# Performance work log

Hardware: AMD Instinct MI355X
Metric: run time of the kernel (lower is better)

The kernel has to match this reference:

```python
import jax, jax.numpy as jnp
import numpy as np

N, E, D, C = 50000, 800000, 128, 7
BN_EPS = 1e-5


def _sage_conv(x, src, dst, Wl, Wr, b):
    # mean-aggregate neighbor messages per destination, then linear + root linear
    msgs = x[src]  # [E, D] irregular gather
    summed = jax.ops.segment_sum(msgs, dst, num_segments=N)
    cnt = jax.ops.segment_sum(jnp.ones((src.shape[0],), x.dtype), dst, num_segments=N)
    agg = summed / jnp.maximum(cnt, 1.0)[:, None]
    return agg @ Wl.T + x @ Wr.T + b


def _bn_eval(x, g, be):
    # running_mean=0, running_var=1 (eval mode)
    return x * (g / jnp.sqrt(1.0 + BN_EPS)) + be


def setup_inputs() -> dict:
    key = jax.random.key(0)
    ks = jax.random.split(key, 20)
    w = lambda k, s: jax.random.normal(k, s, dtype=jnp.float32) * 0.05
    inp = {
        "x": jax.random.normal(ks[0], (N, D), dtype=jnp.float32),
        "edge_index": jax.random.randint(ks[1], (2, E), 0, N, dtype=jnp.int64),
        "Wl0": w(ks[2], (D, D)), "Wr0": w(ks[3], (D, D)), "b0": jnp.zeros((D,), jnp.float32),
        "Wl1": w(ks[4], (D, D)), "Wr1": w(ks[5], (D, D)), "b1": jnp.zeros((D,), jnp.float32),
        "Wl2": w(ks[6], (D, D)), "Wr2": w(ks[7], (D, D)), "b2": jnp.zeros((D,), jnp.float32),
        "g0": jnp.ones((D,), jnp.float32), "be0": jnp.zeros((D,), jnp.float32),
        "g1": jnp.ones((D,), jnp.float32), "be1": jnp.zeros((D,), jnp.float32),
        "dW1": w(ks[8], (D, D)), "db1": jnp.zeros((D,), jnp.float32),
        "dW2": w(ks[9], (C, D)), "db2": jnp.zeros((C,), jnp.float32),
        "dW3": w(ks[10], (D, D)), "db3": jnp.zeros((D,), jnp.float32),
    }
    return inp


def reference(x, edge_index, Wl0, Wr0, b0, Wl1, Wr1, b1, Wl2, Wr2, b2,
              g0, be0, g1, be1, dW1, db1, dW2, db2, dW3, db3):
    src, dst = edge_index[0], edge_index[1]
    h = _sage_conv(x, src, dst, Wl0, Wr0, b0)
    h = jax.nn.relu(_bn_eval(h, g0, be0))  # dropout is identity in eval
    h = _sage_conv(h, src, dst, Wl1, Wr1, b1)
    h = jax.nn.relu(_bn_eval(h, g1, be1))
    h = _sage_conv(h, src, dst, Wl2, Wr2, b2)
    recon_x1 = h @ dW1.T + db1
    recon_x2 = h @ dW2.T + db2
    recon_x3 = h @ dW3.T + db3
    return (recon_x1, recon_x2, recon_x3)
```

## Files before the change

kernel.cpp:

```cpp
#include <hip/hip_runtime.h>
#include <hip/hip_fp16.h>

static constexpr float kBnEps = 1e-5f;
static constexpr int MAXB = 1024;

typedef __attribute__((ext_vector_type(8))) _Float16 f16x8;
typedef __attribute__((ext_vector_type(4))) float f32x4;

__global__ void detect_k(const int* __restrict__ eb, int* __restrict__ flag) {
    int l = threadIdx.x;
    int v = eb[2 * l + 1];
    unsigned long long m = __ballot(v == 0);
    if (l == 0) flag[0] = (m == ~0ull) ? 1 : 0;
}

__device__ __forceinline__ int edge_src(const int* eb, int is64, int E, int e) {
    return is64 ? eb[2 * e] : eb[e];
}
__device__ __forceinline__ int edge_dst(const int* eb, int is64, int E, int e) {
    return is64 ? eb[2 * E + 2 * e] : eb[E + e];
}

__global__ __launch_bounds__(256) void histA_k(const int* __restrict__ eb,
                                               const int* __restrict__ flag,
                                               int* __restrict__ gcnt, int E,
                                               int nbuck) {
    __shared__ int lh[MAXB];
    for (int i = threadIdx.x; i < nbuck; i += 256) lh[i] = 0;
    __syncthreads();
    int is64 = flag[0];
    int base = blockIdx.x * 4096;
#pragma unroll
    for (int i = 0; i < 16; ++i) {
        int e = base + i * 256 + threadIdx.x;
        if (e < E) {
            int d = edge_dst(eb, is64, E, e);
            atomicAdd(&lh[d >> 7], 1);
        }
    }
    __syncthreads();
    for (int i = threadIdx.x; i < nbuck; i += 256) {
        int c = lh[i];
        if (c) atomicAdd(&gcnt[i], c);
    }
}

__global__ __launch_bounds__(512) void scanB_k(const int* __restrict__ gcnt,
                                               int* __restrict__ gbase,
                                               int* __restrict__ gcur,
                                               int* __restrict__ offs, int E,
                                               int n, int nbuck) {
    __shared__ int s[512];
    int tid = threadIdx.x;
    int v = (tid < nbuck) ? gcnt[tid] : 0;
    s[tid] = v;
    __syncthreads();
    for (int d = 1; d < 512; d <<= 1) {
        int t = (tid >= d) ? s[tid - d] : 0;
        __syncthreads();
        s[tid] += t;
        __syncthreads();
    }
    if (tid < nbuck) {
        gbase[tid] = s[tid] - v;
        gcur[tid] = s[tid] - v;
    }
    if (tid == 0) {
        gbase[nbuck] = E;
        offs[n] = E;
    }
}

__global__ __launch_bounds__(256) void binC_k(const int* __restrict__ eb,
                                              const int* __restrict__ flag,
                                              int* __restrict__ gcur,
                                              unsigned* __restrict__ bins, int E,
                                              int nbuck) {
    __shared__ int lh[MAXB];
    __shared__ int lcur[MAXB];
    for (int i = threadIdx.x; i < nbuck; i += 256) lh[i] = 0;
    __syncthreads();
    int is64 = flag[0];
    int base = blockIdx.x * 4096;
    int ds[16], ss[16];
#pragma unroll
    for (int i = 0; i < 16; ++i) {
        int e = base + i * 256 + threadIdx.x;
        ds[i] = -1;
        if (e < E) {
            ds[i] = edge_dst(eb, is64, E, e);
            ss[i] = edge_src(eb, is64, E, e);
            atomicAdd(&lh[ds[i] >> 7], 1);
        }
    }
    __syncthreads();
    for (int b = threadIdx.x; b < nbuck; b += 256) {
        int c = lh[b];
        lcur[b] = c ? atomicAdd(&gcur[b], c) : 0;
    }
    __syncthreads();
#pragma unroll
    for (int i = 0; i < 16; ++i) {
        if (ds[i] >= 0) {
            int bkt = ds[i] >> 7;
            int p = atomicAdd(&lcur[bkt], 1);
            bins[p] = ((unsigned)ss[i] << 7) | (unsigned)(ds[i] & 127);
        }
    }
}

__global__ __launch_bounds__(256) void csrD_k(const unsigned* __restrict__ bins,
                                              const int* __restrict__ gbase,
                                              int* __restrict__ offs,
                                              int* __restrict__ csr, int n) {
    int b = blockIdx.x;
    __shared__ int hist[128];
    __shared__ int s[128];
    __shared__ int cur[128];
    int tid = threadIdx.x;
    if (tid < 128) hist[tid] = 0;
    __syncthreads();
    int base = gbase[b], endb = gbase[b + 1], m = endb - base;
    for (int i = tid; i < m; i += 256) atomicAdd(&hist[bins[base + i] & 127u], 1);
    __syncthreads();
    int v = 0;
    if (tid < 128) {
        v = hist[tid];
        s[tid] = v;
    }
    __syncthreads();
    for (int d = 1; d < 128; d <<= 1) {
        int t = (tid >= d && tid < 128) ? s[tid - d] : 0;
        __syncthreads();
        if (tid < 128) s[tid] += t;
        __syncthreads();
    }
    if (tid < 128) {
        int excl = s[tid] - v;
        int dst = b * 128 + tid;
        if (dst < n) offs[dst] = base + excl;
        cur[tid] = base + excl;
    }
    __syncthreads();
    for (int i = tid; i < m; i += 256) {
        unsigned u = bins[base + i];
        int p = atomicAdd(&cur[u & 127u], 1);
        csr[p] = (int)(u >> 7);
    }
}

__global__ void cvtx_k(const float* __restrict__ in, __half* __restrict__ out, int total8) {
    int i = blockIdx.x * blockDim.x + threadIdx.x;
    if (i >= total8) return;
    float4 v0 = ((const float4*)in)[2 * i];
    float4 v1 = ((const float4*)in)[2 * i + 1];
    __half2 h0 = __floats2half2_rn(v0.x, v0.y);
    __half2 h1 = __floats2half2_rn(v0.z, v0.w);
    __half2 h2 = __floats2half2_rn(v1.x, v1.y);
    __half2 h3 = __floats2half2_rn(v1.z, v1.w);
    uint4 o;
    o.x = *(uint*)&h0; o.y = *(uint*)&h1; o.z = *(uint*)&h2; o.w = *(uint*)&h3;
    ((uint4*)out)[i] = o;
}

__global__ void cvtw_k(const float* __restrict__ Wl0, const float* __restrict__ Wr0,
                       const float* __restrict__ Wl1, const float* __restrict__ Wr1,
                       const float* __restrict__ Wl2, const float* __restrict__ Wr2,
                       const float* __restrict__ dW1, const float* __restrict__ dW3,
                       __half* __restrict__ Wcat, __half* __restrict__ dWcat) {
    int idx = blockIdx.x * 256 + threadIdx.x;
    if (idx < 3 * 32768) {
        int l = idx >> 15;
        int rem = idx & 32767;
        int nn = rem >> 8;
        int k = rem & 255;
        const float* Wl = (l == 0) ? Wl0 : (l == 1) ? Wl1 : Wl2;
        const float* Wr = (l == 0) ? Wr0 : (l == 1) ? Wr1 : Wr2;
        float v = (k < 128) ? Wl[nn * 128 + k] : Wr[nn * 128 + (k - 128)];
        Wcat[idx] = __float2half_rn(v);
    } else if (idx < 3 * 32768 + 16384) {
        int j = idx - 3 * 32768;
        dWcat[j] = __float2half_rn(dW1[j]);
    } else if (idx < 3 * 32768 + 32768) {
        int j = idx - 3 * 32768 - 16384;
        dWcat[16384 + j] = __float2half_rn(dW3[j]);
    }
}

__global__ void agg_k(const __half* __restrict__ Xh, const int* __restrict__ offs,
                      const int* __restrict__ csr, __half* __restrict__ aggh, int n) {
    int gt = blockIdx.x * blockDim.x + threadIdx.x;
    int wid = gt >> 6;
    int lane = threadIdx.x & 63;
    if (wid >= n) return;
    int beg = offs[wid], end = offs[wid + 1];
    int len = end - beg;
    const uint* Xp = (const uint*)Xh;
    float a0 = 0.f, a1 = 0.f;
    for (int j0 = 0; j0 < len; j0 += 8) {
        int idx[8];
        float w[8];
#pragma unroll
        for (int t = 0; t < 8; ++t) {
            int jj = j0 + t;
            bool ok = jj < len;
            idx[t] = csr[beg + (ok ? jj : 0)];
            w[t] = ok ? 1.f : 0.f;
        }
        uint v[8];
#pragma unroll
        for (int t = 0; t < 8; ++t)
            v[t] = Xp[(size_t)idx[t] * 64 + lane];
#pragma unroll
        for (int t = 0; t < 8; ++t) {
            __half2 h = *(__half2*)&v[t];
            a0 += w[t] * __low2float(h);
            a1 += w[t] * __high2float(h);
        }
    }
    float inv = 1.0f / fmaxf((float)len, 1.0f);
    __half2 o = __floats2half2_rn(a0 * inv, a1 * inv);
    ((uint*)aggh)[(size_t)wid * 64 + lane] = *(uint*)&o;
}

template <int KTOT, bool TWO_SRC, bool BN_RELU, bool OUT16>
__global__ __launch_bounds__(256) void mgemm_k(
    const __half* __restrict__ A0, const __half* __restrict__ A1,
    const __half* __restrict__ Bw, const float* __restrict__ bias,
    const float* __restrict__ g, const float* __restrict__ be,
    void* __restrict__ outv, const float* __restrict__ bias2,
    void* __restrict__ outv2, int n) {
    constexpr int ROWB = KTOT * 2 + 16;
    __shared__ char sA[128 * ROWB];

    if (blockIdx.y == 1) {
        Bw += 128 * KTOT;
        bias = bias2;
        outv = outv2;
    }

    const int tid = threadIdx.x;
    const int lane = tid & 63;
    const int wid = tid >> 6;
    const int wm = wid & 1;
    const int wn = wid >> 1;
    const int row0 = blockIdx.x * 128;

    constexpr int CPR = KTOT / 8;
#pragma unroll
    for (int i = 0; i < (128 * CPR) / 256; ++i) {
        int idx = tid + i * 256;
        int r = idx / CPR;
        int c = idx % CPR;
        int rg = row0 + r;
        float4 v = make_float4(0.f, 0.f, 0.f, 0.f);
        if (rg < n) {
            if (TWO_SRC)
                v = (c < 16) ? *(const float4*)(A0 + (size_t)rg * 128 + c * 8)
                             : *(const float4*)(A1 + (size_t)rg * 128 + (c - 16) * 8);
            else
                v = *(const float4*)(A0 + (size_t)rg * 128 + c * 8);
        }
        *(float4*)(&sA[r * ROWB + c * 16]) = v;
    }

    f32x4 acc[4][4];
#pragma unroll
    for (int mi = 0; mi < 4; ++mi)
#pragma unroll
        for (int ni = 0; ni < 4; ++ni) acc[mi][ni] = (f32x4){0.f, 0.f, 0.f, 0.f};

    __syncthreads();

    const int bcol = wn * 64;
    constexpr int KH = KTOT / 128;
#pragma unroll
    for (int kh = 0; kh < KH; ++kh) {
        f16x8 bfr[4][4];
#pragma unroll
        for (int ni = 0; ni < 4; ++ni)
#pragma unroll
            for (int kt = 0; kt < 4; ++kt) {
                int col = bcol + ni * 16 + (lane & 15);
                int ko = kh * 128 + kt * 32 + (lane >> 4) * 8;
                bfr[ni][kt] = *(const f16x8*)(Bw + (size_t)col * KTOT + ko);
            }
#pragma unroll
        for (int mi = 0; mi < 4; ++mi) {
            int rl = wm * 64 + mi * 16 + (lane & 15);
            const char* base = &sA[rl * ROWB + kh * 256 + (lane >> 4) * 16];
            f16x8 afr[4];
#pragma unroll
            for (int kt = 0; kt < 4; ++kt) afr[kt] = *(const f16x8*)(base + kt * 64);
#pragma unroll
            for (int kt = 0; kt < 4; ++kt)
#pragma unroll
                for (int ni = 0; ni < 4; ++ni)
                    acc[mi][ni] = __builtin_amdgcn_mfma_f32_16x16x32_f16(
                        afr[kt], bfr[ni][kt], acc[mi][ni], 0, 0, 0);
        }
    }

#pragma unroll
    for (int ni = 0; ni < 4; ++ni) {
        int col = bcol + ni * 16 + (lane & 15);
        float bv = bias[col];
        float gs = 0.f, bes = 0.f;
        if (BN_RELU) {
            gs = g[col] / sqrtf(1.0f + kBnEps);
            bes = be[col];
        }
#pragma unroll
        for (int mi = 0; mi < 4; ++mi) {
#pragma unroll
            for (int r = 0; r < 4; ++r) {
                int row = row0 + wm * 64 + mi * 16 + (lane >> 4) * 4 + r;
                if (row < n) {
                    float v = acc[mi][ni][r] + bv;
                    if (BN_RELU) v = fmaxf(v * gs + bes, 0.f);
                    if (OUT16)
                        ((__half*)outv)[(size_t)row * 128 + col] = __float2half_rn(v);
                    else
                        ((float*)outv)[(size_t)row * 128 + col] = v;
                }
            }
        }
    }
}

__global__ __launch_bounds__(256) void head2_k(const __half* __restrict__ h,
                                               const float* __restrict__ W2,
                                               const float* __restrict__ b2,
                                               float* __restrict__ out, int n) {
    __shared__ float sw[7 * 128];
    __shared__ float sb[7];
    int tid = threadIdx.x;
    for (int i = tid; i < 7 * 128; i += 256) sw[i] = W2[i];
    if (tid < 7) sb[tid] = b2[tid];
    __syncthreads();
    int row = blockIdx.x * 256 + tid;
    if (row >= n) return;
    const uint4* hr = (const uint4*)(h + (size_t)row * 128);
    float acc[7] = {0.f, 0.f, 0.f, 0.f, 0.f, 0.f, 0.f};
    for (int q = 0; q < 16; ++q) {
        uint4 u = hr[q];
        const __half2* p = (const __half2*)&u;
        float f[8];
#pragma unroll
        for (int t = 0; t < 4; ++t) {
            f[2 * t] = __low2float(p[t]);
            f[2 * t + 1] = __high2float(p[t]);
        }
#pragma unroll
        for (int c = 0; c < 7; ++c)
#pragma unroll
            for (int j = 0; j < 8; ++j) acc[c] += f[j] * sw[c * 128 + q * 8 + j];
    }
#pragma unroll
    for (int c = 0; c < 7; ++c) out[(size_t)row * 7 + c] = acc[c] + sb[c];
}

extern "C" void kernel_launch(void* const* d_in, const int* in_sizes, int n_in,
                              void* d_out, int out_size, void* d_ws, size_t ws_size,
                              hipStream_t stream) {
    const float* x   = (const float*)d_in[0];
    const int*   eb  = (const int*)d_in[1];
    const float* Wl0 = (const float*)d_in[2];
    const float* Wr0 = (const float*)d_in[3];
    const float* b0  = (const float*)d_in[4];
    const float* Wl1 = (const float*)d_in[5];
    const float* Wr1 = (const float*)d_in[6];
    const float* b1  = (const float*)d_in[7];
    const float* Wl2 = (const float*)d_in[8];
    const float* Wr2 = (const float*)d_in[9];
    const float* b2  = (const float*)d_in[10];
    const float* g0  = (const float*)d_in[11];
    const float* be0 = (const float*)d_in[12];
    const float* g1  = (const float*)d_in[13];
    const float* be1 = (const float*)d_in[14];
    const float* dW1 = (const float*)d_in[15];
    const float* db1 = (const float*)d_in[16];
    const float* dW2 = (const float*)d_in[17];
    const float* db2 = (const float*)d_in[18];
    const float* dW3 = (const float*)d_in[19];
    const float* db3 = (const float*)d_in[20];

    const int n = in_sizes[0] / 128;
    const int E = in_sizes[1] / 2;
    const int nbuck = (n + 127) >> 7;

    char* ws = (char*)d_ws;
    size_t off = 0;
    auto alloc = [&](size_t bytes) -> void* {
        void* p = ws + off;
        off = (off + bytes + 255) & ~(size_t)255;
        return p;
    };
    int*      flag  = (int*)alloc(16);
    int*      gcnt  = (int*)alloc(MAXB * 4);
    int*      gbase = (int*)alloc((MAXB + 1) * 4);
    int*      gcur  = (int*)alloc(MAXB * 4);
    unsigned* bins  = (unsigned*)alloc((size_t)E * 4);
    int*      csr   = (int*)alloc((size_t)E * 4);
    int*      offs  = (int*)alloc((size_t)(n + 1) * 4);
    __half*   x_h   = (__half*)alloc((size_t)n * 128 * 2);
    __half*   agg_h = (__half*)alloc((size_t)n * 128 * 2);
    __half*   h0    = (__half*)alloc((size_t)n * 128 * 2);
    __half*   h1    = (__half*)alloc((size_t)n * 128 * 2);
    __half*   h2    = h0;
    __half*   Wcat  = (__half*)alloc(3 * 32768 * 2);
    __half*   dWcat = (__half*)alloc(32768 * 2);

    float* out0 = (float*)d_out;
    float* out1 = out0 + (size_t)n * 128;
    float* out2 = out1 + (size_t)n * 7;

    hipMemsetAsync(gcnt, 0, MAXB * 4, stream);

    const int nbN = (n + 255) / 256;
    const int ggrid = (n + 127) / 128;
    const int agg_grid = (n * 64 + 255) / 256;
    const int chunk_grid = (E + 4095) / 4096;

    detect_k<<<1, 64, 0, stream>>>(eb, flag);
    histA_k<<<chunk_grid, 256, 0, stream>>>(eb, flag, gcnt, E, nbuck);
    scanB_k<<<1, 512, 0, stream>>>(gcnt, gbase, gcur, offs, E, n, nbuck);
    binC_k<<<chunk_grid, 256, 0, stream>>>(eb, flag, gcur, bins, E, nbuck);
    csrD_k<<<nbuck, 256, 0, stream>>>(bins, gbase, offs, csr, n);

    cvtx_k<<<(n * 16 + 255) / 256, 256, 0, stream>>>(x, x_h, n * 16);
    cvtw_k<<<(131072 + 255) / 256, 256, 0, stream>>>(Wl0, Wr0, Wl1, Wr1, Wl2, Wr2,
                                                     dW1, dW3, Wcat, dWcat);

    agg_k<<<agg_grid, 256, 0, stream>>>(x_h, offs, csr, agg_h, n);
    mgemm_k<256, true, true, true><<<ggrid, 256, 0, stream>>>(
        agg_h, x_h, Wcat, b0, g0, be0, h0, nullptr, nullptr, n);
    agg_k<<<agg_grid, 256, 0, stream>>>(h0, offs, csr, agg_h, n);
    mgemm_k<256, true, true, true><<<ggrid, 256, 0, stream>>>(
        agg_h, h0, Wcat + 32768, b1, g1, be1, h1, nullptr, nullptr, n);
    agg_k<<<agg_grid, 256, 0, stream>>>(h1, offs, csr, agg_h, n);
    mgemm_k<256, true, false, true><<<ggrid, 256, 0, stream>>>(
        agg_h, h1, Wcat + 65536, b2, nullptr, nullptr, h2, nullptr, nullptr, n);
    mgemm_k<128, false, false, false><<<dim3(ggrid, 2), 256, 0, stream>>>(
        h2, nullptr, dWcat, db1, nullptr, nullptr, out0, db3, out2, n);
    head2_k<<<nbN, 256, 0, stream>>>(h2, dW2, db2, out1, n);
}
```

Baseline: 253.9 us.

## Vectorize neighbor aggregation across lane groups and fuse class head into GEMM

Aggregation now splits each wavefront into four 16-lane groups, each lane loading 8 halves per neighbor, so 32 neighbors are gathered per iteration and reduced with cross-lane shuffles. This aims to raise memory-level parallelism and use wider loads in the gather-bound step. The 7-class head is folded into the output GEMM as a third grid slice with a zero-padded weight block, removing a separate scalar kernel at the cost of wasted MFMA columns.

```diff
diff --git a/kernel.cpp b/kernel.cpp
--- a/kernel.cpp
+++ b/kernel.cpp
@@ -167,6 +167,7 @@
                        const float* __restrict__ Wl1, const float* __restrict__ Wr1,
                        const float* __restrict__ Wl2, const float* __restrict__ Wr2,
                        const float* __restrict__ dW1, const float* __restrict__ dW3,
+                       const float* __restrict__ dW2,
                        __half* __restrict__ Wcat, __half* __restrict__ dWcat) {
     int idx = blockIdx.x * 256 + threadIdx.x;
     if (idx < 3 * 32768) {
@@ -178,65 +179,86 @@
         const float* Wr = (l == 0) ? Wr0 : (l == 1) ? Wr1 : Wr2;
         float v = (k < 128) ? Wl[nn * 128 + k] : Wr[nn * 128 + (k - 128)];
         Wcat[idx] = __float2half_rn(v);
-    } else if (idx < 3 * 32768 + 16384) {
+    } else if (idx < 3 * 32768 + 3 * 16384) {
         int j = idx - 3 * 32768;
-        dWcat[j] = __float2half_rn(dW1[j]);
-    } else if (idx < 3 * 32768 + 32768) {
-        int j = idx - 3 * 32768 - 16384;
-        dWcat[16384 + j] = __float2half_rn(dW3[j]);
-    }
-}
-
-__global__ void agg_k(const __half* __restrict__ Xh, const int* __restrict__ offs,
-                      const int* __restrict__ csr, __half* __restrict__ aggh, int n) {
+        int blk = j >> 14;
+        int r = (j & 16383) >> 7;
+        int c = j & 127;
+        float v;
+        if (blk == 0) v = dW1[r * 128 + c];
+        else if (blk == 1) v = dW3[r * 128 + c];
+        else v = (r < 7) ? dW2[r * 128 + c] : 0.f;
+        dWcat[j] = __float2half_rn(v);
+    }
+}
+
+__global__ __launch_bounds__(256) void agg_k(const __half* __restrict__ Xh,
+                                             const int* __restrict__ offs,
+                                             const int* __restrict__ csr,
+                                             __half* __restrict__ aggh, int n) {
     int gt = blockIdx.x * blockDim.x + threadIdx.x;
-    int wid = gt >> 6;
+    int node = gt >> 6;
     int lane = threadIdx.x & 63;
-    if (wid >= n) return;
-    int beg = offs[wid], end = offs[wid + 1];
+    int grp = lane >> 4;
+    int lg = lane & 15;
+    if (node >= n) return;
+    int beg = offs[node], end = offs[node + 1];
     int len = end - beg;
-    const uint* Xp = (const uint*)Xh;
-    float a0 = 0.f, a1 = 0.f;
-    for (int j0 = 0; j0 < len; j0 += 8) {
-        int idx[8];
-        float w[8];
+    const f16x8* Xp = (const f16x8*)Xh;
+    float acc[8];
+#pragma unroll
+    for (int k = 0; k < 8; ++k) acc[k] = 0.f;
+    for (int j0 = 0; j0 < len; j0 += 32) {
+        int jj[8];
+        bool ok[8];
+        f16x8 v[8];
 #pragma unroll
         for (int t = 0; t < 8; ++t) {
-            int jj = j0 + t;
-            bool ok = jj < len;
-            idx[t] = csr[beg + (ok ? jj : 0)];
-            w[t] = ok ? 1.f : 0.f;
-        }
-        uint v[8];
+            int j = j0 + grp * 8 + t;
+            ok[t] = j < len;
+            jj[t] = csr[beg + (ok[t] ? j : 0)];
+        }
 #pragma unroll
         for (int t = 0; t < 8; ++t)
-            v[t] = Xp[(size_t)idx[t] * 64 + lane];
-#pragma unroll
-        for (int t = 0; t < 8; ++t) {
-            __half2 h = *(__half2*)&v[t];
-            a0 += w[t] * __low2float(h);
-            a1 += w[t] * __high2float(h);
-        }
-    }
-    float inv = 1.0f / fmaxf((float)len, 1.0f);
-    __half2 o = __floats2half2_rn(a0 * inv, a1 * inv);
-    ((uint*)aggh)[(size_t)wid * 64 + lane] = *(uint*)&o;
-}
-
-template <int KTOT, bool TWO_SRC, bool BN_RELU, bool OUT16>
+            if (ok[t]) v[t] = Xp[(size_t)jj[t] * 16 + lg];
+#pragma unroll
+        for (int t = 0; t < 8; ++t)
+            if (ok[t]) {
+#pragma unroll
+                for (int k = 0; k < 8; ++k) acc[k] += (float)v[t][k];
+            }
+    }
+#pragma unroll
+    for (int k = 0; k < 8; ++k) {
+        acc[k] += __shfl_xor(acc[k], 16, 64);
+        acc[k] += __shfl_xor(acc[k], 32, 64);
+    }
+    if (grp == 0) {
+        float inv = 1.0f / fmaxf((float)len, 1.0f);
+        f16x8 o;
+#pragma unroll
+        for (int k = 0; k < 8; ++k) o[k] = (_Float16)(acc[k] * inv);
+        ((f16x8*)aggh)[(size_t)node * 16 + lg] = o;
+    }
+}
+
+template <int KTOT, bool TWO_SRC, bool BN_RELU, bool OUT16, bool HEADS>
 __global__ __launch_bounds__(256) void mgemm_k(
     const __half* __restrict__ A0, const __half* __restrict__ A1,
     const __half* __restrict__ Bw, const float* __restrict__ bias,
     const float* __restrict__ g, const float* __restrict__ be,
     void* __restrict__ outv, const float* __restrict__ bias2,
-    void* __restrict__ outv2, int n) {
+    void* __restrict__ outv2, const float* __restrict__ bias3,
+    void* __restrict__ outv3, int n) {
     constexpr int ROWB = KTOT * 2 + 16;
     __shared__ char sA[128 * ROWB];
 
-    if (blockIdx.y == 1) {
-        Bw += 128 * KTOT;
-        bias = bias2;
-        outv = outv2;
+    int ncol = 128, ostride = 128;
+    if (HEADS) {
+        int y = blockIdx.y;
+        Bw += (size_t)y * 128 * KTOT;
+        if (y == 1) { bias = bias2; outv = outv2; }
+        if (y == 2) { bias = bias3; outv = outv3; ncol = 7; ostride = 7; }
     }
 
     const int tid = threadIdx.x;
@@ -304,6 +326,7 @@
 #pragma unroll
     for (int ni = 0; ni < 4; ++ni) {
         int col = bcol + ni * 16 + (lane & 15);
+        if (HEADS && col >= ncol) continue;
         float bv = bias[col];
         float gs = 0.f, bes = 0.f;
         if (BN_RELU) {
@@ -321,43 +344,11 @@
                     if (OUT16)
                         ((__half*)outv)[(size_t)row * 128 + col] = __float2half_rn(v);
                     else
-                        ((float*)outv)[(size_t)row * 128 + col] = v;
+                        ((float*)outv)[(size_t)row * ostride + col] = v;
                 }
             }
         }
     }
-}
-
-__global__ __launch_bounds__(256) void head2_k(const __half* __restrict__ h,
-                                               const float* __restrict__ W2,
-                                               const float* __restrict__ b2,
-                                               float* __restrict__ out, int n) {
-    __shared__ float sw[7 * 128];
-    __shared__ float sb[7];
-    int tid = threadIdx.x;
-    for (int i = tid; i < 7 * 128; i += 256) sw[i] = W2[i];
-    if (tid < 7) sb[tid] = b2[tid];
-    __syncthreads();
-    int row = blockIdx.x * 256 + tid;
-    if (row >= n) return;
-    const uint4* hr = (const uint4*)(h + (size_t)row * 128);
-    float acc[7] = {0.f, 0.f, 0.f, 0.f, 0.f, 0.f, 0.f};
-    for (int q = 0; q < 16; ++q) {
-        uint4 u = hr[q];
-        const __half2* p = (const __half2*)&u;
-        float f[8];
-#pragma unroll
-        for (int t = 0; t < 4; ++t) {
-            f[2 * t] = __low2float(p[t]);
-            f[2 * t + 1] = __high2float(p[t]);
-        }
-#pragma unroll
-        for (int c = 0; c < 7; ++c)
-#pragma unroll
-            for (int j = 0; j < 8; ++j) acc[c] += f[j] * sw[c * 128 + q * 8 + j];
-    }
-#pragma unroll
-    for (int c = 0; c < 7; ++c) out[(size_t)row * 7 + c] = acc[c] + sb[c];
 }
 
 extern "C" void kernel_launch(void* const* d_in, const int* in_sizes, int n_in,
@@ -409,7 +400,7 @@
     __half*   h1    = (__half*)alloc((size_t)n * 128 * 2);
     __half*   h2    = h0;
     __half*   Wcat  = (__half*)alloc(3 * 32768 * 2);
-    __half*   dWcat = (__half*)alloc(32768 * 2);
+    __half*   dWcat = (__half*)alloc(3 * 16384 * 2);
 
     float* out0 = (float*)d_out;
     float* out1 = out0 + (size_t)n * 128;
@@ -417,7 +408,6 @@
 
     hipMemsetAsync(gcnt, 0, MAXB * 4, stream);
 
-    const int nbN = (n + 255) / 256;
     const int ggrid = (n + 127) / 128;
     const int agg_grid = (n * 64 + 255) / 256;
     const int chunk_grid = (E + 4095) / 4096;
@@ -429,19 +419,19 @@
     csrD_k<<<nbuck, 256, 0, stream>>>(bins, gbase, offs, csr, n);
 
     cvtx_k<<<(n * 16 + 255) / 256, 256, 0, stream>>>(x, x_h, n * 16);
-    cvtw_k<<<(131072 + 255) / 256, 256, 0, stream>>>(Wl0, Wr0, Wl1, Wr1, Wl2, Wr2,
-                                                     dW1, dW3, Wcat, dWcat);
+    cvtw_k<<<(147456 + 255) / 256, 256, 0, stream>>>(Wl0, Wr0, Wl1, Wr1, Wl2, Wr2,
+                                                     dW1, dW3, dW2, Wcat, dWcat);
 
     agg_k<<<agg_grid, 256, 0, stream>>>(x_h, offs, csr, agg_h, n);
-    mgemm_k<256, true, true, true><<<ggrid, 256, 0, stream>>>(
-        agg_h, x_h, Wcat, b0, g0, be0, h0, nullptr, nullptr, n);
+    mgemm_k<256, true, true, true, false><<<ggrid, 256, 0, stream>>>(
+        agg_h, x_h, Wcat, b0, g0, be0, h0, nullptr, nullptr, nullptr, nullptr, n);
     agg_k<<<agg_grid, 256, 0, stream>>>(h0, offs, csr, agg_h, n);
-    mgemm_k<256, true, true, true><<<ggrid, 256, 0, stream>>>(
-        agg_h, h0, Wcat + 32768, b1, g1, be1, h1, nullptr, nullptr, n);
+    mgemm_k<256, true, true, true, false><<<ggrid, 256, 0, stream>>>(
+        agg_h, h0, Wcat + 32768, b1, g1, be1, h1, nullptr, nullptr, nullptr, nullptr, n);
     agg_k<<<agg_grid, 256, 0, stream>>>(h1, offs, csr, agg_h, n);
-    mgemm_k<256, true, false, true><<<ggrid, 256, 0, stream>>>(
-        agg_h, h1, Wcat + 65536, b2, nullptr, nullptr, h2, nullptr, nullptr, n);
-    mgemm_k<128, false, false, false><<<dim3(ggrid, 2), 256, 0, stream>>>(
-        h2, nullptr, dWcat, db1, nullptr, nullptr, out0, db3, out2, n);
-    head2_k<<<nbN, 256, 0, stream>>>(h2, dW2, db2, out1, n);
-}
+    mgemm_k<256, true, false, true, false><<<ggrid, 256, 0, stream>>>(
+        agg_h, h1, Wcat + 65536, b2, nullptr, nullptr, h2, nullptr, nullptr, nullptr,
+        nullptr, n);
+    mgemm_k<128, false, false, false, true><<<dim3(ggrid, 3), 256, 0, stream>>>(
+        h2, nullptr, dWcat, db1, nullptr, nullptr, out0, db3, out2, db2, out1, n);
+}
```

After: 265.5 us. 4.6% more time.
